# Optimization experiments

Measured on AMD Instinct MI355X. Metric: run time of the kernel, lower is better.

The kernel has to match this reference:

```python
import math
import jax, jax.numpy as jnp
import numpy as np

NUM_HEADS = 12
ALPHA, BETA, GAMMA = 1.9, 3.8, 15.2  # get_rpe_config(ratio=1.9)
SKIP = 1


def _rp_bucket(side):
    """iRPE euclidean contextual bucket table for a side x side grid + 1 cls token."""
    beta_int = int(BETA)
    coords = np.stack(np.meshgrid(np.arange(side), np.arange(side), indexing='ij'), -1).reshape(-1, 2)
    diff = coords[:, None, :] - coords[None, :, :]
    dis = np.round(np.sqrt((diff ** 2).sum(-1).astype(np.float64)))  # rounded euclidean distance
    far = np.clip(np.round(ALPHA + np.log(np.maximum(dis, 1e-9) / ALPHA) / math.log(GAMMA / ALPHA) * (BETA - ALPHA)), None, BETA)
    idx = np.where(dis <= ALPHA, dis, far).astype(np.int32) + beta_int
    num_buckets = 2 * beta_int + 1  # 7
    L = side * side
    full = np.full((L + SKIP, L + SKIP), num_buckets, dtype=np.int32)  # extra bucket for cls
    full[SKIP:, SKIP:] = idx
    return full, num_buckets + 1  # table [P,P], total buckets = 8


def setup_inputs() -> dict:
    key = jax.random.key(0)
    ks = jax.random.split(key, 8)
    B, P, n_mod, C = 64, 197, 2, 768
    N = 1 + (P - 1) * n_mod  # 393
    hd = C // NUM_HEADS
    rp_bucket, n_buckets = _rp_bucket(int(math.sqrt(P - SKIP)))
    s = 0.02
    return {
        'x': jax.random.normal(ks[0], (B, N, C), jnp.float32),
        'q_learned': jax.random.normal(ks[1], (1, 1, C), jnp.float32) * s,
        'pos_embed': jax.random.normal(ks[2], (1, P, C), jnp.float32) * s,
        'wk': jax.random.normal(ks[3], (C, C), jnp.float32) * s,
        'wv': jax.random.normal(ks[4], (C, C), jnp.float32) * s,
        'rpe_w': jax.random.normal(ks[5], (hd, n_buckets), jnp.float32) * s,  # shared_head ctx lookup table
        'proj_w': jax.random.normal(ks[6], (C, C), jnp.float32) * s,
        'proj_b': jnp.zeros((C,), jnp.float32),
        'rp_bucket': jnp.asarray(rp_bucket),  # [P, P] int32
    }


def reference(x, q_learned, pos_embed, wk, wv, rpe_w, proj_w, proj_b, rp_bucket):
    B, N, C = x.shape
    H = NUM_HEADS
    hd = C // H
    P = rp_bucket.shape[0]
    n_mod = (N - 1) // (P - 1)
    scale = hd ** -0.5

    q_ = jnp.broadcast_to(q_learned + pos_embed, (B, P, C))
    q = q_.reshape(B, P, H, hd).transpose(0, 2, 1, 3)                    # bhpd
    k = (x @ wk.T).reshape(B, N, H, hd).transpose(0, 2, 1, 3)            # bhnd
    v = (x @ wv.T).reshape(B, N, H, hd).transpose(0, 2, 1, 3)            # bhnd

    attn = jnp.einsum('bhpd,bhnd->bhpn', q, k) * scale                   # [B,H,P,N]

    # contextual RPE on keys: lookup = q @ table, gathered by rp_bucket[i, j]
    lookup = jnp.einsum('bhpd,du->bhpu', q, rpe_w)                        # [B,H,P,n_buckets]
    bias = lookup[:, :, jnp.arange(P)[:, None], rp_bucket]                # [B,H,P,P]
    bias = jnp.concatenate([bias[..., :1], jnp.tile(bias[..., 1:], (1, 1, 1, n_mod))], axis=-1)
    attn = jax.nn.softmax(attn + bias, axis=-1)

    out = jnp.einsum('bhpn,bhnd->bhpd', attn, v).transpose(0, 2, 1, 3).reshape(B, P, C)
    return out @ proj_w.T + proj_b
```

## Files before the change

### kernel.cpp

```cpp
#include <hip/hip_runtime.h>

typedef unsigned short u16;
typedef short bf16x8 __attribute__((ext_vector_type(8)));
typedef float f32x4 __attribute__((ext_vector_type(4)));
typedef const __attribute__((address_space(1))) void* gptr_t;
typedef __attribute__((address_space(3))) void* lptr_t;

#define B_   64
#define N_   393
#define C_   768
#define H_   12
#define HD_  64
#define P_   197
#define BIAS_N 416
#define PPAD 208
#define VTP  448
#define M_KV (B_ * N_)
#define M_PR (B_ * P_)
#define SCALE_L2E 0.180336879f

__device__ __forceinline__ u16 f2bf(float f) {
    unsigned u = __float_as_uint(f);
    return (u16)((u + 0x7FFFu + ((u >> 16) & 1u)) >> 16);
}
__device__ __forceinline__ unsigned cvt_pk_bf16(float lo, float hi) {
    unsigned r;
    asm("v_cvt_pk_bf16_f32 %0, %1, %2" : "=v"(r) : "v"(lo), "v"(hi));
    return r;
}
__device__ __forceinline__ float exp2_fast(float x) {
    float r;
    asm("v_exp_f32 %0, %1" : "=v"(r) : "v"(x));
    return r;
}

__global__ __launch_bounds__(256) void conv_all(
    const float* __restrict__ x, const float* __restrict__ wk,
    const float* __restrict__ wv, const float* __restrict__ pw,
    u16* __restrict__ xh, u16* __restrict__ wkvh, u16* __restrict__ pwh)
{
    const int XN4 = 19316736 / 4;
    const int WN4 = 589824 / 4;
    int i = blockIdx.x * 256 + threadIdx.x;
    const float* src; u16* dst; int off;
    if (i < XN4) { src = x; dst = xh; off = i; }
    else {
        int j = i - XN4;
        int sec = j / WN4;
        off = j - sec * WN4;
        src = sec == 0 ? wk : (sec == 1 ? wv : pw);
        dst = sec == 0 ? wkvh : (sec == 1 ? wkvh + 589824 : pwh);
    }
    float4 v = ((const float4*)src)[off];
    u16 o[4] = {f2bf(v.x), f2bf(v.y), f2bf(v.z), f2bf(v.w)};
    *(uint2*)(dst + off * 4) = *(uint2*)o;
}

__global__ __launch_bounds__(256) void prep1_kernel(
    const float* __restrict__ q_learned, const float* __restrict__ pos_embed,
    const float* __restrict__ rpe_w, u16* __restrict__ qh, float* __restrict__ lk)
{
    __shared__ float q_s[C_];
    const int p = blockIdx.x, t = threadIdx.x;
    for (int c = t; c < C_; c += 256) {
        float v = q_learned[c] + pos_embed[p * C_ + c];
        q_s[c] = v;
        qh[p * C_ + c] = f2bf(v);
    }
    __syncthreads();
    if (t < H_ * 8) {
        int h = t >> 3, u = t & 7;
        float s = 0.f;
        #pragma unroll 8
        for (int d = 0; d < HD_; ++d)
            s = fmaf(q_s[h * HD_ + d], rpe_w[d * 8 + u], s);
        lk[(h * P_ + p) * 8 + u] = s;
    }
}

__global__ __launch_bounds__(256) void prep2_kernel(
    const float* __restrict__ lk, const int* __restrict__ rp_bucket,
    float* __restrict__ biasT)
{
    int bx = blockIdx.x;
    int h = bx / N_, j = bx % N_;
    int t = threadIdx.x;
    if (t >= PPAD) return;
    int jm;
    if (j == 0) jm = 0;
    else { jm = j - 1; if (jm >= 196) jm -= 196; jm += 1; }
    float v = 0.f;
    if (t < P_) {
        int bucket = rp_bucket[t * P_ + jm];
        v = lk[(h * P_ + t) * 8 + bucket] * 1.44269504f;
    }
    biasT[((size_t)h * BIAS_N + j) * PPAD + t] = v;
}

template <bool F32OUT>
__global__ __launch_bounds__(256) void gemm_bf16(
    const u16* __restrict__ A, const u16* __restrict__ Bw,
    u16* __restrict__ Cb, float* __restrict__ Cf, const float* __restrict__ bias,
    int M, int ldc)
{
    __shared__ __align__(16) u16 As[128 * 64];
    __shared__ __align__(16) u16 Bs[128 * 64];

    const int gx = gridDim.x;
    const int nwg = gx * gridDim.y;
    const int orig = blockIdx.y * gx + blockIdx.x;
    const int xcd = orig & 7, rank = orig >> 3;
    const int q = nwg >> 3, r = nwg & 7;
    const int wgid = (xcd < r ? xcd * (q + 1) : r * (q + 1) + (xcd - r) * q) + rank;
    const int n0 = (wgid % gx) * 128;
    const int m0 = (wgid / gx) * 128;

    const int t = threadIdx.x;
    const int w = t >> 6, l = t & 63;
    const int wr = w >> 1, wc = w & 1;
    const int l15 = l & 15, lg = l >> 4;
    const int lrow = l >> 3, lslot = l & 7;
    const int Mc = M - 1;

    f32x4 acc[4][4];
    #pragma unroll
    for (int i = 0; i < 4; ++i)
        #pragma unroll
        for (int j = 0; j < 4; ++j) acc[i][j] = (f32x4){0.f, 0.f, 0.f, 0.f};

    for (int ks = 0; ks < 12; ++ks) {
        const int k0 = ks * 64;
        if (ks) __syncthreads();
        #pragma unroll
        for (int i = 0; i < 4; ++i) {
            const int rbase = w * 32 + i * 8;
            int arow = m0 + rbase + lrow; if (arow > Mc) arow = Mc;
            const int brow = n0 + rbase + lrow;
            const u16* ga = A  + (size_t)arow * 768 + k0 + lslot * 8;
            const u16* gb = Bw + (size_t)brow * 768 + k0 + lslot * 8;
            __builtin_amdgcn_global_load_lds((gptr_t)(const void*)ga,
                                             (lptr_t)(void*)(As + rbase * 64), 16, 0, 0);
            __builtin_amdgcn_global_load_lds((gptr_t)(const void*)gb,
                                             (lptr_t)(void*)(Bs + rbase * 64), 16, 0, 0);
        }
        __syncthreads();
        #pragma unroll
        for (int kk = 0; kk < 2; ++kk) {
            bf16x8 af[4], bfr[4];
            #pragma unroll
            for (int mf = 0; mf < 4; ++mf) {
                af[mf]  = *(const bf16x8*)(As + (wr * 64 + mf * 16 + l15) * 64 + (kk * 4 + lg) * 8);
                bfr[mf] = *(const bf16x8*)(Bs + (wc * 64 + mf * 16 + l15) * 64 + (kk * 4 + lg) * 8);
            }
            #pragma unroll
            for (int mf = 0; mf < 4; ++mf)
                #pragma unroll
                for (int nf = 0; nf < 4; ++nf)
                    acc[mf][nf] = __builtin_amdgcn_mfma_f32_16x16x32_bf16(
                        af[mf], bfr[nf], acc[mf][nf], 0, 0, 0);
        }
    }

    #pragma unroll
    for (int mf = 0; mf < 4; ++mf) {
        #pragma unroll
        for (int nf = 0; nf < 4; ++nf) {
            int col = n0 + wc * 64 + nf * 16 + l15;
            float bb = 0.f;
            if (F32OUT) bb = bias[col];
            #pragma unroll
            for (int rr = 0; rr < 4; ++rr) {
                int m = m0 + wr * 64 + mf * 16 + lg * 4 + rr;
                if (m < M) {
                    if (F32OUT) Cf[(size_t)m * ldc + col] = acc[mf][nf][rr] + bb;
                    else        Cb[(size_t)m * ldc + col] = f2bf(acc[mf][nf][rr]);
                }
            }
        }
    }
}

__global__ __launch_bounds__(256) void vtrans_kernel(const u16* __restrict__ KV,
                                                     u16* __restrict__ Vt)
{
    const int bh = blockIdx.x;
    const int b = bh / H_, h = bh % H_;
    const int t = threadIdx.x, w = t >> 6, l = t & 63;
    const int d = w * 16 + (l >> 2);
    const int c = l & 3;
    const u16* src = KV + (size_t)b * N_ * 1536 + 768 + h * HD_ + d;
    u16* dst = Vt + (size_t)(bh * HD_ + d) * VTP;
    for (int jb = 0; jb < VTP; jb += 32) {
        int j0 = jb + c * 8;
        u16 v[8];
        #pragma unroll
        for (int i = 0; i < 8; ++i) {
            int j = j0 + i;
            v[i] = (j < N_) ? src[(size_t)j * 1536] : (u16)0;
        }
        *(bf16x8*)(dst + j0) = *(bf16x8*)v;
    }
}

__global__ __launch_bounds__(256, 2) void attn_mfma5(
    const u16* __restrict__ qh, const u16* __restrict__ KV,
    const u16* __restrict__ Vt, const float* __restrict__ biasT,
    u16* __restrict__ Obuf)
{
    __shared__ __align__(16) u16 pts[64 * 456];
    __shared__ __align__(16) u16 kvs[2][64 * 64];

    const int id = blockIdx.x;
    const int work = (id & 7) * 384 + (id >> 3);
    const int ptile = work & 3;
    const int rest = work >> 2;
    const int h = rest % 12;
    const int b = rest / 12;
    const int p0 = ptile * 64;

    const int t = threadIdx.x, w = t >> 6, l = t & 63;
    const int l15 = l & 15, lg = l >> 4;
    const int p0w = p0 + w * 16;

    int srow[2], sslot[2], swoff[2];
    #pragma unroll
    for (int i = 0; i < 2; ++i) {
        int c = t + 256 * i;
        srow[i] = c >> 3; sslot[i] = c & 7;
        swoff[i] = srow[i] * 64 + ((sslot[i] ^ (srow[i] & 7)) << 3);
    }

    int prow = p0w + l15; if (prow > P_ - 1) prow = P_ - 1;
    const u16* qp = qh + (size_t)prow * C_ + h * HD_ + lg * 8;
    bf16x8 qf0 = *(const bf16x8*)(qp);
    bf16x8 qf1 = *(const bf16x8*)(qp + 32);

    const u16* Kbase = KV + (size_t)b * (N_ * 1536) + h * HD_;
    const u16* Vbase = Vt + (size_t)(b * H_ + h) * (HD_ * VTP);

    f32x4 acc[7][4];
    #pragma unroll
    for (int i = 0; i < 7; ++i)
        #pragma unroll
        for (int j = 0; j < 4; ++j) acc[i][j] = (f32x4){0.f, 0.f, 0.f, 0.f};

    bf16x8 ra[2];
    #pragma unroll
    for (int i = 0; i < 2; ++i)
        ra[i] = *(const bf16x8*)(Kbase + (size_t)srow[i] * 1536 + sslot[i] * 8);
    #pragma unroll
    for (int i = 0; i < 2; ++i) *(bf16x8*)(&kvs[0][swoff[i]]) = ra[i];
    __syncthreads();

    #pragma unroll
    for (int nt = 0; nt < 7; ++nt) {
        const u16* kcur = kvs[nt & 1];
        if (nt < 6) {
            #pragma unroll
            for (int i = 0; i < 2; ++i) {
                int rn = (nt + 1) * 64 + srow[i]; if (rn > N_ - 1) rn = N_ - 1;
                ra[i] = *(const bf16x8*)(Kbase + (size_t)rn * 1536 + sslot[i] * 8);
            }
        }
        const int smax = (nt == 6) ? 1 : 4;
        __builtin_amdgcn_s_setprio(1);
        #pragma unroll
        for (int kc = 0; kc < 2; ++kc)
            #pragma unroll
            for (int sub = 0; sub < smax; ++sub) {
                int row = sub * 16 + l15;
                bf16x8 kb = *(const bf16x8*)(kcur + row * 64 + (((kc * 4 + lg) ^ (row & 7)) << 3));
                acc[nt][sub] = __builtin_amdgcn_mfma_f32_16x16x32_bf16(
                    kc ? qf1 : qf0, kb, acc[nt][sub], 0, 0, 0);
            }
        __builtin_amdgcn_s_setprio(0);
        if (nt < 6) {
            #pragma unroll
            for (int i = 0; i < 2; ++i) *(bf16x8*)(&kvs[(nt + 1) & 1][swoff[i]]) = ra[i];
        }
        __syncthreads();
    }

    #pragma unroll
    for (int i = 0; i < 2; ++i)
        ra[i] = *(const bf16x8*)(Vbase + (size_t)srow[i] * VTP + sslot[i] * 8);

    const int pcl = (p0w + lg * 4) > (PPAD - 4) ? (PPAD - 4) : (p0w + lg * 4);
    float s4[4] = {0.f, 0.f, 0.f, 0.f};
    #pragma unroll
    for (int nt = 0; nt < 7; ++nt) {
        const int smax = (nt == 6) ? 1 : 4;
        #pragma unroll
        for (int sub = 0; sub < smax; ++sub) {
            int n = nt * 64 + sub * 16 + l15;
            if (n < N_) {
                float4 b4 = *(const float4*)(biasT + ((size_t)h * BIAS_N + n) * PPAD + pcl);
                float bb[4] = {b4.x, b4.y, b4.z, b4.w};
                #pragma unroll
                for (int rr = 0; rr < 4; ++rr) {
                    float e = exp2_fast(fmaf(acc[nt][sub][rr], SCALE_L2E, bb[rr]));
                    acc[nt][sub][rr] = e;
                    s4[rr] += e;
                }
            } else {
                acc[nt][sub] = (f32x4){0.f, 0.f, 0.f, 0.f};
            }
        }
    }
    float rinv4[4];
    #pragma unroll
    for (int rr = 0; rr < 4; ++rr) {
        float s = s4[rr];
        s += __shfl_xor(s, 1); s += __shfl_xor(s, 2);
        s += __shfl_xor(s, 4); s += __shfl_xor(s, 8);
        rinv4[rr] = 1.0f / s;
    }

    {
        const int rowb = w * 16 + lg * 4;
        #pragma unroll
        for (int nt = 0; nt < 7; ++nt) {
            const int smax = (nt == 6) ? 1 : 4;
            #pragma unroll
            for (int sub = 0; sub < smax; ++sub) {
                int col = nt * 64 + sub * 16 + l15;
                unsigned pk01 = cvt_pk_bf16(acc[nt][sub][0], acc[nt][sub][1]);
                unsigned pk23 = cvt_pk_bf16(acc[nt][sub][2], acc[nt][sub][3]);
                pts[(rowb + 0) * 456 + col] = (u16)pk01;
                pts[(rowb + 1) * 456 + col] = (u16)(pk01 >> 16);
                pts[(rowb + 2) * 456 + col] = (u16)pk23;
                pts[(rowb + 3) * 456 + col] = (u16)(pk23 >> 16);
            }
        }
        #pragma unroll
        for (int rr = 0; rr < 4; ++rr)
            pts[(rowb + rr) * 456 + 400 + l15] = 0;
    }
    #pragma unroll
    for (int i = 0; i < 2; ++i) *(bf16x8*)(&kvs[0][swoff[i]]) = ra[i];
    __syncthreads();

    f32x4 o[4];
    #pragma unroll
    for (int i = 0; i < 4; ++i) o[i] = (f32x4){0.f, 0.f, 0.f, 0.f};

    #pragma unroll
    for (int nt = 0; nt < 7; ++nt) {
        const u16* kcur = kvs[nt & 1];
        if (nt < 6) {
            #pragma unroll
            for (int i = 0; i < 2; ++i)
                ra[i] = *(const bf16x8*)(Vbase + (size_t)srow[i] * VTP + (nt + 1) * 64 + sslot[i] * 8);
        }
        const int kcmax = (nt == 6) ? 1 : 2;
        __builtin_amdgcn_s_setprio(1);
        #pragma unroll
        for (int kc = 0; kc < kcmax; ++kc) {
            bf16x8 pa = *(const bf16x8*)(pts + (w * 16 + l15) * 456 + nt * 64 + kc * 32 + lg * 8);
            #pragma unroll
            for (int dsub = 0; dsub < 4; ++dsub) {
                int row = dsub * 16 + l15;
                bf16x8 vb = *(const bf16x8*)(kcur + row * 64 + (((kc * 4 + lg) ^ (row & 7)) << 3));
                o[dsub] = __builtin_amdgcn_mfma_f32_16x16x32_bf16(pa, vb, o[dsub], 0, 0, 0);
            }
        }
        __builtin_amdgcn_s_setprio(0);
        if (nt < 6) {
            #pragma unroll
            for (int i = 0; i < 2; ++i) *(bf16x8*)(&kvs[(nt + 1) & 1][swoff[i]]) = ra[i];
        }
        __syncthreads();
    }

    #pragma unroll
    for (int dsub = 0; dsub < 4; ++dsub)
        #pragma unroll
        for (int rr = 0; rr < 4; ++rr) {
            int p = p0w + lg * 4 + rr;
            if (p < P_)
                Obuf[((size_t)b * P_ + p) * C_ + h * HD_ + dsub * 16 + l15] =
                    f2bf(o[dsub][rr] * rinv4[rr]);
        }
}

extern "C" void kernel_launch(void* const* d_in, const int* in_sizes, int n_in,
                              void* d_out, int out_size, void* d_ws, size_t ws_size,
                              hipStream_t stream)
{
    const float* x         = (const float*)d_in[0];
    const float* q_learned = (const float*)d_in[1];
    const float* pos_embed = (const float*)d_in[2];
    const float* wk        = (const float*)d_in[3];
    const float* wv        = (const float*)d_in[4];
    const float* rpe_w     = (const float*)d_in[5];
    const float* proj_w    = (const float*)d_in[6];
    const float* proj_b    = (const float*)d_in[7];
    const int*   rp_bucket = (const int*)d_in[8];
    float* out = (float*)d_out;

    char* ws = (char*)d_ws;
    u16*   xh    = (u16*)(ws);
    u16*   wkvh  = (u16*)(ws + 38633472);
    u16*   pwh   = (u16*)(ws + 40992768);
    u16*   qh    = (u16*)(ws + 42172416);
    float* lk    = (float*)(ws + 42475008);
    float* biasT = (float*)(ws + 42550784);
    u16*   KV    = (u16*)(ws + 46704128);
    u16*   Vt    = (u16*)(ws + 123971072);
    u16*   Obuf  = (u16*)(ws + 168011264);

    conv_all<<<20592, 256, 0, stream>>>(x, wk, wv, proj_w, xh, wkvh, pwh);

    prep1_kernel<<<P_, 256, 0, stream>>>(q_learned, pos_embed, rpe_w, qh, lk);
    prep2_kernel<<<H_ * N_, 256, 0, stream>>>(lk, rp_bucket, biasT);

    dim3 gkv(1536 / 128, (M_KV + 127) / 128);
    gemm_bf16<false><<<gkv, 256, 0, stream>>>(xh, wkvh, KV, nullptr, nullptr, M_KV, 1536);

    vtrans_kernel<<<B_ * H_, 256, 0, stream>>>(KV, Vt);

    attn_mfma5<<<3072, 256, 0, stream>>>(qh, KV, Vt, biasT, Obuf);

    dim3 gpr(768 / 128, (M_PR + 127) / 128);
    gemm_bf16<true><<<gpr, 256, 0, stream>>>(Obuf, pwh, nullptr, out, proj_b, M_PR, 768);
}
```

Measured before the change: 239.1 us.

## Double-buffer LDS in bf16 GEMM with prefetch two k-tiles ahead

Restructures the projection GEMM main loop into a double-buffered LDS pipeline. Global-to-LDS loads for k-tile ks+2 are issued right after the fragments of tile ks are read into registers, and explicit vmcnt waits and barriers replace the load-then-sync pattern. The loop is fully unrolled, per-row pointers are hoisted, MFMA priority is raised with setprio, and launch bounds request two blocks per CU. LDS use doubles to 64KB per block, which can limit occupancy, and the vmcnt counts depend on exactly 8 loads per stage.

Result: slower. 248.5 us (+4.0%).

```diff
diff --git a/kernel.cpp b/kernel.cpp
--- a/kernel.cpp
+++ b/kernel.cpp
@@ -98,13 +98,13 @@
 }
 
 template <bool F32OUT>
-__global__ __launch_bounds__(256) void gemm_bf16(
+__global__ __launch_bounds__(256, 2) void gemm_bf16(
     const u16* __restrict__ A, const u16* __restrict__ Bw,
     u16* __restrict__ Cb, float* __restrict__ Cf, const float* __restrict__ bias,
     int M, int ldc)
 {
-    __shared__ __align__(16) u16 As[128 * 64];
-    __shared__ __align__(16) u16 Bs[128 * 64];
+    __shared__ __align__(16) u16 As[2][8192];
+    __shared__ __align__(16) u16 Bs[2][8192];
 
     const int gx = gridDim.x;
     const int nwg = gx * gridDim.y;
@@ -122,44 +122,74 @@
     const int lrow = l >> 3, lslot = l & 7;
     const int Mc = M - 1;
 
+    const u16* gA[4]; const u16* gB[4];
+    #pragma unroll
+    for (int i = 0; i < 4; ++i) {
+        const int rbase = w * 32 + i * 8;
+        int arow = m0 + rbase + lrow; if (arow > Mc) arow = Mc;
+        gA[i] = A + (size_t)arow * 768 + lslot * 8;
+        gB[i] = Bw + (size_t)(n0 + rbase + lrow) * 768 + lslot * 8;
+    }
+
     f32x4 acc[4][4];
     #pragma unroll
     for (int i = 0; i < 4; ++i)
         #pragma unroll
         for (int j = 0; j < 4; ++j) acc[i][j] = (f32x4){0.f, 0.f, 0.f, 0.f};
 
-    for (int ks = 0; ks < 12; ++ks) {
-        const int k0 = ks * 64;
-        if (ks) __syncthreads();
-        #pragma unroll
-        for (int i = 0; i < 4; ++i) {
-            const int rbase = w * 32 + i * 8;
-            int arow = m0 + rbase + lrow; if (arow > Mc) arow = Mc;
-            const int brow = n0 + rbase + lrow;
-            const u16* ga = A  + (size_t)arow * 768 + k0 + lslot * 8;
-            const u16* gb = Bw + (size_t)brow * 768 + k0 + lslot * 8;
-            __builtin_amdgcn_global_load_lds((gptr_t)(const void*)ga,
-                                             (lptr_t)(void*)(As + rbase * 64), 16, 0, 0);
-            __builtin_amdgcn_global_load_lds((gptr_t)(const void*)gb,
-                                             (lptr_t)(void*)(Bs + rbase * 64), 16, 0, 0);
-        }
-        __syncthreads();
-        #pragma unroll
-        for (int kk = 0; kk < 2; ++kk) {
-            bf16x8 af[4], bfr[4];
-            #pragma unroll
-            for (int mf = 0; mf < 4; ++mf) {
-                af[mf]  = *(const bf16x8*)(As + (wr * 64 + mf * 16 + l15) * 64 + (kk * 4 + lg) * 8);
-                bfr[mf] = *(const bf16x8*)(Bs + (wc * 64 + mf * 16 + l15) * 64 + (kk * 4 + lg) * 8);
-            }
-            #pragma unroll
-            for (int mf = 0; mf < 4; ++mf)
-                #pragma unroll
-                for (int nf = 0; nf < 4; ++nf)
-                    acc[mf][nf] = __builtin_amdgcn_mfma_f32_16x16x32_bf16(
-                        af[mf], bfr[nf], acc[mf][nf], 0, 0, 0);
-        }
-    }
+#define STAGE(KT, DB) do {                                                      \
+    _Pragma("unroll") for (int _i = 0; _i < 4; ++_i) {                          \
+        const int _rb = w * 32 + _i * 8;                                        \
+        __builtin_amdgcn_global_load_lds((gptr_t)(const void*)(gA[_i] + (KT) * 64), \
+            (lptr_t)(void*)(&As[DB][_rb * 64]), 16, 0, 0);                      \
+        __builtin_amdgcn_global_load_lds((gptr_t)(const void*)(gB[_i] + (KT) * 64), \
+            (lptr_t)(void*)(&Bs[DB][_rb * 64]), 16, 0, 0);                      \
+    }                                                                           \
+} while (0)
+
+#define GITER(KS, VM, DOSTG) do {                                               \
+    asm volatile("s_waitcnt vmcnt(" #VM ")" ::: "memory");                      \
+    __builtin_amdgcn_s_barrier();                                               \
+    const int _db = (KS) & 1;                                                   \
+    bf16x8 _af[8], _bf[8];                                                      \
+    _Pragma("unroll") for (int _kk = 0; _kk < 2; ++_kk)                         \
+        _Pragma("unroll") for (int _mf = 0; _mf < 4; ++_mf) {                   \
+            _af[_kk * 4 + _mf] = *(const bf16x8*)(                              \
+                &As[_db][(wr * 64 + _mf * 16 + l15) * 64 + (_kk * 4 + lg) * 8]);\
+            _bf[_kk * 4 + _mf] = *(const bf16x8*)(                              \
+                &Bs[_db][(wc * 64 + _mf * 16 + l15) * 64 + (_kk * 4 + lg) * 8]);\
+        }                                                                       \
+    asm volatile("s_waitcnt lgkmcnt(0)" ::: "memory");                          \
+    __builtin_amdgcn_s_barrier();                                               \
+    if (DOSTG) { STAGE((KS) + 2, _db); }                                        \
+    __builtin_amdgcn_sched_barrier(0);                                          \
+    __builtin_amdgcn_s_setprio(1);                                              \
+    _Pragma("unroll") for (int _kk = 0; _kk < 2; ++_kk)                         \
+        _Pragma("unroll") for (int _mf = 0; _mf < 4; ++_mf)                     \
+            _Pragma("unroll") for (int _nf = 0; _nf < 4; ++_nf)                 \
+                acc[_mf][_nf] = __builtin_amdgcn_mfma_f32_16x16x32_bf16(        \
+                    _af[_kk * 4 + _mf], _bf[_kk * 4 + _nf], acc[_mf][_nf], 0, 0, 0); \
+    __builtin_amdgcn_s_setprio(0);                                              \
+} while (0)
+
+    STAGE(0, 0);
+    STAGE(1, 1);
+
+    GITER(0, 8, 1);
+    GITER(1, 8, 1);
+    GITER(2, 8, 1);
+    GITER(3, 8, 1);
+    GITER(4, 8, 1);
+    GITER(5, 8, 1);
+    GITER(6, 8, 1);
+    GITER(7, 8, 1);
+    GITER(8, 8, 1);
+    GITER(9, 8, 1);
+    GITER(10, 8, 0);
+    GITER(11, 0, 0);
+
+#undef GITER
+#undef STAGE
 
     #pragma unroll
     for (int mf = 0; mf < 4; ++mf) {
```

## Merge prep kernels into conversion and V-transpose launches; tile V transpose through LDS

Applied to the files above, without the earlier changes.

Folds the q/lookup prep into the bf16 conversion launch and the bias-table build into the V-transpose launch, cutting two kernel launches. The V transpose now does coalesced 16-byte row loads into an LDS tile and writes transposed vectors. Before, each thread gathered strided scalar loads. This aims to cut launch overhead and uncoalesced global reads, at the cost of extra block-size branching and LDS sync.

Result: faster. 228.0 us (-4.6%).

```diff
diff --git a/kernel.cpp b/kernel.cpp
--- a/kernel.cpp
+++ b/kernel.cpp
@@ -34,67 +34,49 @@
     return r;
 }
 
-__global__ __launch_bounds__(256) void conv_all(
+__global__ __launch_bounds__(256) void conv_prep1(
     const float* __restrict__ x, const float* __restrict__ wk,
     const float* __restrict__ wv, const float* __restrict__ pw,
-    u16* __restrict__ xh, u16* __restrict__ wkvh, u16* __restrict__ pwh)
-{
-    const int XN4 = 19316736 / 4;
-    const int WN4 = 589824 / 4;
-    int i = blockIdx.x * 256 + threadIdx.x;
-    const float* src; u16* dst; int off;
-    if (i < XN4) { src = x; dst = xh; off = i; }
-    else {
-        int j = i - XN4;
-        int sec = j / WN4;
-        off = j - sec * WN4;
-        src = sec == 0 ? wk : (sec == 1 ? wv : pw);
-        dst = sec == 0 ? wkvh : (sec == 1 ? wkvh + 589824 : pwh);
-    }
-    float4 v = ((const float4*)src)[off];
-    u16 o[4] = {f2bf(v.x), f2bf(v.y), f2bf(v.z), f2bf(v.w)};
-    *(uint2*)(dst + off * 4) = *(uint2*)o;
-}
-
-__global__ __launch_bounds__(256) void prep1_kernel(
     const float* __restrict__ q_learned, const float* __restrict__ pos_embed,
-    const float* __restrict__ rpe_w, u16* __restrict__ qh, float* __restrict__ lk)
+    const float* __restrict__ rpe_w,
+    u16* __restrict__ xh, u16* __restrict__ wkvh, u16* __restrict__ pwh,
+    u16* __restrict__ qh, float* __restrict__ lk)
 {
     __shared__ float q_s[C_];
-    const int p = blockIdx.x, t = threadIdx.x;
-    for (int c = t; c < C_; c += 256) {
-        float v = q_learned[c] + pos_embed[p * C_ + c];
-        q_s[c] = v;
-        qh[p * C_ + c] = f2bf(v);
-    }
-    __syncthreads();
-    if (t < H_ * 8) {
-        int h = t >> 3, u = t & 7;
-        float s = 0.f;
-        #pragma unroll 8
-        for (int d = 0; d < HD_; ++d)
-            s = fmaf(q_s[h * HD_ + d], rpe_w[d * 8 + u], s);
-        lk[(h * P_ + p) * 8 + u] = s;
-    }
-}
-
-__global__ __launch_bounds__(256) void prep2_kernel(
-    const float* __restrict__ lk, const int* __restrict__ rp_bucket,
-    float* __restrict__ biasT)
-{
-    int bx = blockIdx.x;
-    int h = bx / N_, j = bx % N_;
-    int t = threadIdx.x;
-    if (t >= PPAD) return;
-    int jm;
-    if (j == 0) jm = 0;
-    else { jm = j - 1; if (jm >= 196) jm -= 196; jm += 1; }
-    float v = 0.f;
-    if (t < P_) {
-        int bucket = rp_bucket[t * P_ + jm];
-        v = lk[(h * P_ + t) * 8 + bucket] * 1.44269504f;
-    }
-    biasT[((size_t)h * BIAS_N + j) * PPAD + t] = v;
+    const int bx = blockIdx.x, t = threadIdx.x;
+    if (bx < 20592) {
+        const int XN4 = 19316736 / 4;
+        const int WN4 = 589824 / 4;
+        int i = bx * 256 + t;
+        const float* src; u16* dst; int off;
+        if (i < XN4) { src = x; dst = xh; off = i; }
+        else {
+            int j = i - XN4;
+            int sec = j / WN4;
+            off = j - sec * WN4;
+            src = sec == 0 ? wk : (sec == 1 ? wv : pw);
+            dst = sec == 0 ? wkvh : (sec == 1 ? wkvh + 589824 : pwh);
+        }
+        float4 v = ((const float4*)src)[off];
+        u16 o[4] = {f2bf(v.x), f2bf(v.y), f2bf(v.z), f2bf(v.w)};
+        *(uint2*)(dst + off * 4) = *(uint2*)o;
+    } else {
+        const int p = bx - 20592;
+        for (int c = t; c < C_; c += 256) {
+            float v = q_learned[c] + pos_embed[p * C_ + c];
+            q_s[c] = v;
+            qh[p * C_ + c] = f2bf(v);
+        }
+        __syncthreads();
+        if (t < H_ * 8) {
+            int h = t >> 3, u = t & 7;
+            float s = 0.f;
+            #pragma unroll 8
+            for (int d = 0; d < HD_; ++d)
+                s = fmaf(q_s[h * HD_ + d], rpe_w[d * 8 + u], s);
+            lk[(h * P_ + p) * 8 + u] = s;
+        }
+    }
 }
 
 template <bool F32OUT>
@@ -180,25 +162,53 @@
     }
 }
 
-__global__ __launch_bounds__(256) void vtrans_kernel(const u16* __restrict__ KV,
-                                                     u16* __restrict__ Vt)
+__global__ __launch_bounds__(256) void vtrans_prep2(
+    const u16* __restrict__ KV, u16* __restrict__ Vt,
+    const float* __restrict__ lk, const int* __restrict__ rp_bucket,
+    float* __restrict__ biasT)
 {
-    const int bh = blockIdx.x;
-    const int b = bh / H_, h = bh % H_;
-    const int t = threadIdx.x, w = t >> 6, l = t & 63;
-    const int d = w * 16 + (l >> 2);
-    const int c = l & 3;
-    const u16* src = KV + (size_t)b * N_ * 1536 + 768 + h * HD_ + d;
-    u16* dst = Vt + (size_t)(bh * HD_ + d) * VTP;
-    for (int jb = 0; jb < VTP; jb += 32) {
-        int j0 = jb + c * 8;
-        u16 v[8];
-        #pragma unroll
-        for (int i = 0; i < 8; ++i) {
-            int j = j0 + i;
-            v[i] = (j < N_) ? src[(size_t)j * 1536] : (u16)0;
-        }
-        *(bf16x8*)(dst + j0) = *(bf16x8*)v;
+    __shared__ __align__(16) u16 vts[64][68];
+    const int bx = blockIdx.x, t = threadIdx.x;
+    if (bx < B_ * H_) {
+        const int b = bx / H_, h = bx % H_;
+        const u16* src = KV + (size_t)b * N_ * 1536 + 768 + h * HD_;
+        u16* dst = Vt + (size_t)bx * HD_ * VTP;
+        for (int jt = 0; jt < 7; ++jt) {
+            const int j0 = jt * 64;
+            if (jt) __syncthreads();
+            #pragma unroll
+            for (int ps = 0; ps < 2; ++ps) {
+                int jr = ps * 32 + (t >> 3);
+                int dd = (t & 7) * 8;
+                int j = j0 + jr;
+                bf16x8 v = (bf16x8){0, 0, 0, 0, 0, 0, 0, 0};
+                if (j < N_) v = *(const bf16x8*)(src + (size_t)j * 1536 + dd);
+                *(bf16x8*)(&vts[jr][dd]) = v;
+            }
+            __syncthreads();
+            #pragma unroll
+            for (int ps = 0; ps < 2; ++ps) {
+                int idx = t + 256 * ps;
+                int d = idx >> 3, ch = idx & 7;
+                u16 v[8];
+                #pragma unroll
+                for (int k = 0; k < 8; ++k) v[k] = vts[ch * 8 + k][d];
+                *(bf16x8*)(dst + (size_t)d * VTP + j0 + ch * 8) = *(bf16x8*)v;
+            }
+        }
+    } else {
+        const int i = bx - B_ * H_;
+        const int h = i / N_, j = i % N_;
+        if (t >= PPAD) return;
+        int jm;
+        if (j == 0) jm = 0;
+        else { jm = j - 1; if (jm >= 196) jm -= 196; jm += 1; }
+        float v = 0.f;
+        if (t < P_) {
+            int bucket = rp_bucket[t * P_ + jm];
+            v = lk[(h * P_ + t) * 8 + bucket] * 1.44269504f;
+        }
+        biasT[((size_t)h * BIAS_N + j) * PPAD + t] = v;
     }
 }
 
@@ -409,15 +419,14 @@
     u16*   Vt    = (u16*)(ws + 123971072);
     u16*   Obuf  = (u16*)(ws + 168011264);
 
-    conv_all<<<20592, 256, 0, stream>>>(x, wk, wv, proj_w, xh, wkvh, pwh);
-
-    prep1_kernel<<<P_, 256, 0, stream>>>(q_learned, pos_embed, rpe_w, qh, lk);
-    prep2_kernel<<<H_ * N_, 256, 0, stream>>>(lk, rp_bucket, biasT);
+    conv_prep1<<<20789, 256, 0, stream>>>(x, wk, wv, proj_w,
+                                          q_learned, pos_embed, rpe_w,
+                                          xh, wkvh, pwh, qh, lk);
 
     dim3 gkv(1536 / 128, (M_KV + 127) / 128);
     gemm_bf16<false><<<gkv, 256, 0, stream>>>(xh, wkvh, KV, nullptr, nullptr, M_KV, 1536);
 
-    vtrans_kernel<<<B_ * H_, 256, 0, stream>>>(KV, Vt);
+    vtrans_prep2<<<5484, 256, 0, stream>>>(KV, Vt, lk, rp_bucket, biasT);
 
     attn_mfma5<<<3072, 256, 0, stream>>>(qh, KV, Vt, biasT, Obuf);
 
```
